# Kernel optimization log

Hardware: AMD Instinct MI355X
Metric: run time of the kernel (lower is better)

The kernel has to match this reference:

```python
import jax, jax.numpy as jnp
import numpy as np

N = 8192  # batch size
D = 256   # embedding dim


def setup_inputs() -> dict:
    key = jax.random.key(0)
    k1, k2 = jax.random.split(key)
    return {
        "embeddings": jax.random.normal(k1, (N, D), dtype=jnp.float32),
        "query_embeddings": jax.random.normal(k2, (N, D), dtype=jnp.float32),
    }


def _l2_normalize(x, eps=1e-8):
    # matches torch F.cosine_similarity: x / max(||x||, eps)
    n = jnp.sqrt(jnp.sum(x * x, axis=-1, keepdims=True))
    return x / jnp.maximum(n, eps)


def _cross_entropy(logits, targets):
    # mean CE; out-of-range targets clamp to last class (jit gather semantics)
    lse = jax.nn.logsumexp(logits, axis=1)
    t = jnp.clip(targets, 0, logits.shape[1] - 1)
    picked = jnp.take_along_axis(logits, t[:, None], axis=1)[:, 0]
    return jnp.mean(lse - picked)


def reference(embeddings, query_embeddings):
    n = embeddings.shape[0]
    # normalize once, then single NxN matmul (instead of NxNxD broadcast)
    sim = _l2_normalize(embeddings) @ _l2_normalize(query_embeddings).T  # (N, N)
    rows = jnp.arange(n)
    positives = jnp.diagonal(sim)[:, None]  # (N, 1)
    # off-diagonal gather: per row, column indices skipping the diagonal
    idx = jnp.arange(n - 1)
    cols = idx[None, :] + (idx[None, :] >= rows[:, None]).astype(jnp.int32)
    negatives = jnp.take_along_axis(sim, cols, axis=1)  # (N, N-1)
    loss_pos = _cross_entropy(positives, rows)
    loss_neg = _cross_entropy(-negatives, rows)
    return loss_pos + loss_neg
```

## Files before the change

### kernel.cpp

```cpp
#include <hip/hip_runtime.h>
#include <hip/hip_bf16.h>

#define NROWS 8192
#define DIM 256
#define NSPLIT 16
#define JSPAN (NROWS / NSPLIT)
#define NGRP (JSPAN / 16)
#define RPW 64
#define RPB 256
#define GRP_BYTES 8192

typedef __bf16 bf16x8 __attribute__((ext_vector_type(8)));
typedef float f32x4 __attribute__((ext_vector_type(4)));

#define NEG_LOG2E -1.4426950408889634f
#define NEG_LN2   -0.6931471805599453f

__global__ __launch_bounds__(256) void k_normalize_all(const float* __restrict__ emb,
                                                       const float* __restrict__ qry,
                                                       __hip_bfloat16* __restrict__ En,
                                                       __hip_bfloat16* __restrict__ Qn,
                                                       float* __restrict__ rowsum,
                                                       float* __restrict__ out) {
    if (blockIdx.x < 8)
        reinterpret_cast<float4*>(rowsum)[blockIdx.x * 256 + threadIdx.x] =
            float4{0.f, 0.f, 0.f, 0.f};
    if (blockIdx.x == 8 && threadIdx.x == 0) out[0] = 0.f;

    const int gr   = blockIdx.x * 4 + (threadIdx.x >> 6);
    const int lane = threadIdx.x & 63;
    const bool isE = (gr < NROWS);
    const float* in = isE ? emb : qry;
    const int row   = isE ? gr : gr - NROWS;
    const float scale = isE ? NEG_LOG2E : 1.0f;

    const float4 v = reinterpret_cast<const float4*>(in + (size_t)row * DIM)[lane];
    float ss = v.x * v.x + v.y * v.y + v.z * v.z + v.w * v.w;
#pragma unroll
    for (int m = 32; m >= 1; m >>= 1) ss += __shfl_xor(ss, m, 64);
    const float inv = scale / fmaxf(sqrtf(ss), 1e-8f);
    __hip_bfloat16 o[4];
    o[0] = __float2bfloat16(v.x * inv);
    o[1] = __float2bfloat16(v.y * inv);
    o[2] = __float2bfloat16(v.z * inv);
    o[3] = __float2bfloat16(v.w * inv);
    const ushort4 o8 = *reinterpret_cast<const ushort4*>(o);

    if (isE) {
        reinterpret_cast<ushort4*>(En + (size_t)row * DIM)[lane] = o8;
    } else {
        const int g = row >> 4, c = row & 15;
        char* dst = (char*)Qn + (size_t)g * GRP_BYTES
                    + (size_t)(lane >> 3) * 1024 + c * 64 + (lane & 7) * 8;
        *reinterpret_cast<ushort4*>(dst) = o8;
    }
}

__device__ __forceinline__ void stage_group(const char* qlane, char* wdst) {
#pragma unroll
    for (int kk = 0; kk < 8; ++kk)
        __builtin_amdgcn_global_load_lds(
            (const __attribute__((address_space(1))) void*)(qlane + kk * 1024),
            (__attribute__((address_space(3))) void*)(wdst + kk * 1024), 16, 0, 0);
}

__global__ __launch_bounds__(256, 2) void k_simlse(const __hip_bfloat16* __restrict__ En,
                                                   const __hip_bfloat16* __restrict__ Qn,
                                                   float* __restrict__ rowsum,
                                                   float* __restrict__ pickv) {
    __shared__ char lds[4][2][GRP_BYTES];
    const int bx   = blockIdx.x;
    const int ib   = bx >> 4;
    const int jq   = bx & 15;
    const int tid  = threadIdx.x;
    const int lane = tid & 63;
    const int w    = tid >> 6;
    const int l15  = lane & 15;
    const int lks  = lane >> 4;
    const int i0w  = ib * RPB + w * RPW;

    char* wbase = &lds[w][0][0];
    const char* rdbase = wbase + l15 * 64 + lks * 16;

    bf16x8 a[4][8];
    {
        const __hip_bfloat16* ab = En + (size_t)(i0w + l15) * DIM + lks * 8;
#pragma unroll
        for (int mi = 0; mi < 4; ++mi)
#pragma unroll
            for (int kk = 0; kk < 8; ++kk)
                a[mi][kk] = *reinterpret_cast<const bf16x8*>(ab + mi * 16 * DIM + kk * 32);
    }

    float racc[4][4];
#pragma unroll
    for (int mi = 0; mi < 4; ++mi)
#pragma unroll
        for (int r = 0; r < 4; ++r) racc[mi][r] = 0.0f;

    const int jq0 = jq * JSPAN;
    const char* qlane = (const char*)Qn + (size_t)jq0 * 512 + (size_t)lane * 16;
    const char* qnext = qlane + 2 * GRP_BYTES;

    auto step = [&](int p, int rdoff, const char* stsrc) {
        if (p == NGRP - 1) asm volatile("s_waitcnt vmcnt(0)" ::: "memory");
        else               asm volatile("s_waitcnt vmcnt(8)" ::: "memory");

        bf16x8 b[8];
#pragma unroll
        for (int kk = 0; kk < 8; ++kk)
            b[kk] = *reinterpret_cast<const bf16x8*>(rdbase + rdoff + kk * 1024);

        asm volatile("s_waitcnt lgkmcnt(0)" ::: "memory");

        if (p + 2 < NGRP) stage_group(stsrc, wbase + rdoff);

        f32x4 acc[4];
#pragma unroll
        for (int mi = 0; mi < 4; ++mi) acc[mi] = f32x4{0.f, 0.f, 0.f, 0.f};

        __builtin_amdgcn_s_setprio(1);
#pragma unroll
        for (int kk = 0; kk < 8; ++kk)
#pragma unroll
            for (int mi = 0; mi < 4; ++mi)
                acc[mi] = __builtin_amdgcn_mfma_f32_16x16x32_bf16(
                    a[mi][kk], b[kk], acc[mi], 0, 0, 0);
        __builtin_amdgcn_s_setprio(0);

        const int grpbase = jq0 + p * 16;
        const bool spec = (grpbase <= i0w + RPW) && (grpbase + 16 > i0w);
        if (!spec) {
#pragma unroll
            for (int mi = 0; mi < 4; ++mi)
#pragma unroll
                for (int r = 0; r < 4; ++r)
                    racc[mi][r] += __builtin_amdgcn_exp2f(acc[mi][r]);
        } else {
            const int jg = grpbase + l15;
#pragma unroll
            for (int mi = 0; mi < 4; ++mi) {
                const int ig0 = i0w + mi * 16 + lks * 4;
#pragma unroll
                for (int r = 0; r < 4; ++r) {
                    const float e  = __builtin_amdgcn_exp2f(acc[mi][r]);
                    const int   ig = ig0 + r;
                    racc[mi][r] += (jg == ig) ? 0.0f : e;
                    const int pc = (ig == NROWS - 1) ? (NROWS - 2) : (ig + 1);
                    if (jg == pc) pickv[ig] = acc[mi][r] * NEG_LN2;
                }
            }
        }
    };

    stage_group(qlane, wbase);
    stage_group(qlane + GRP_BYTES, wbase + GRP_BYTES);

    for (int pp = 0; pp < NGRP; pp += 2) {
        step(pp,     0,         qnext);
        step(pp + 1, GRP_BYTES, qnext + GRP_BYTES);
        qnext += 2 * GRP_BYTES;
    }

#pragma unroll
    for (int mi = 0; mi < 4; ++mi)
#pragma unroll
        for (int r = 0; r < 4; ++r) {
            float v = racc[mi][r];
            v += __shfl_xor(v, 1, 64);
            v += __shfl_xor(v, 2, 64);
            v += __shfl_xor(v, 4, 64);
            v += __shfl_xor(v, 8, 64);
            if (l15 == 0) atomicAdd(&rowsum[i0w + mi * 16 + lks * 4 + r], v);
        }
}

__global__ __launch_bounds__(256) void k_finalize(const float* __restrict__ rowsum,
                                                  const float* __restrict__ pickv,
                                                  float* __restrict__ out) {
    __shared__ float red[4];
    const int base = blockIdx.x * 512;
    float s = 0.0f;
#pragma unroll
    for (int it = 0; it < 2; ++it) {
        const int i = base + it * 256 + threadIdx.x;
        s += __logf(rowsum[i]) + pickv[i];
    }
#pragma unroll
    for (int m = 32; m >= 1; m >>= 1) s += __shfl_xor(s, m, 64);
    if ((threadIdx.x & 63) == 0) red[threadIdx.x >> 6] = s;
    __syncthreads();
    if (threadIdx.x == 0)
        atomicAdd(out, (red[0] + red[1] + red[2] + red[3]) * (1.0f / (float)NROWS));
}

extern "C" void kernel_launch(void* const* d_in, const int* in_sizes, int n_in,
                              void* d_out, int out_size, void* d_ws, size_t ws_size,
                              hipStream_t stream) {
    const float* emb = (const float*)d_in[0];
    const float* qry = (const float*)d_in[1];
    float* out = (float*)d_out;

    char* ws = (char*)d_ws;
    __hip_bfloat16* En = (__hip_bfloat16*)ws;
    __hip_bfloat16* Qn = (__hip_bfloat16*)(ws + (size_t)NROWS * DIM * 2);
    float* rowsum = (float*)(ws + (size_t)NROWS * DIM * 4);
    float* pickv  = rowsum + NROWS;

    k_normalize_all<<<2 * NROWS / 4, 256, 0, stream>>>(emb, qry, En, Qn, rowsum, out);
    k_simlse<<<32 * NSPLIT, 256, 0, stream>>>(En, Qn, rowsum, pickv);
    k_finalize<<<16, 256, 0, stream>>>(rowsum, pickv, out);
}
```

Measured before the change: 53.55 us.

## Switch similarity GEMM from bf16 to fp8 MFMA with repacked Q layout

Normalized embeddings and queries are now quantized to fp8 instead of bf16, and the similarity GEMM uses the fp8 16x16x32 MFMA. The Q staging layout, LDS group size, column split and occupancy hint are changed to match, and B fragments are now read from LDS inside the MFMA loop rather than preloaded. This halves operand bytes and uses the higher-throughput fp8 matrix path, but the exp of similarities computed from fp8 inputs loses precision, which may push the loss outside tolerance. The grid doubles to 1024 blocks, which adds more atomics on the row sums.

```diff
diff --git a/kernel.cpp b/kernel.cpp
--- a/kernel.cpp
+++ b/kernel.cpp
@@ -3,23 +3,23 @@
 
 #define NROWS 8192
 #define DIM 256
-#define NSPLIT 16
+#define NSPLIT 32
 #define JSPAN (NROWS / NSPLIT)
 #define NGRP (JSPAN / 16)
 #define RPW 64
 #define RPB 256
-#define GRP_BYTES 8192
-
-typedef __bf16 bf16x8 __attribute__((ext_vector_type(8)));
+#define GRP_BYTES 4096
+
 typedef float f32x4 __attribute__((ext_vector_type(4)));
+typedef long i64frag;
 
 #define NEG_LOG2E -1.4426950408889634f
 #define NEG_LN2   -0.6931471805599453f
 
 __global__ __launch_bounds__(256) void k_normalize_all(const float* __restrict__ emb,
                                                        const float* __restrict__ qry,
-                                                       __hip_bfloat16* __restrict__ En,
-                                                       __hip_bfloat16* __restrict__ Qn,
+                                                       unsigned char* __restrict__ En,
+                                                       unsigned char* __restrict__ Qn,
                                                        float* __restrict__ rowsum,
                                                        float* __restrict__ out) {
     if (blockIdx.x < 8)
@@ -39,39 +39,35 @@
 #pragma unroll
     for (int m = 32; m >= 1; m >>= 1) ss += __shfl_xor(ss, m, 64);
     const float inv = scale / fmaxf(sqrtf(ss), 1e-8f);
-    __hip_bfloat16 o[4];
-    o[0] = __float2bfloat16(v.x * inv);
-    o[1] = __float2bfloat16(v.y * inv);
-    o[2] = __float2bfloat16(v.z * inv);
-    o[3] = __float2bfloat16(v.w * inv);
-    const ushort4 o8 = *reinterpret_cast<const ushort4*>(o);
+
+    int pk = __builtin_amdgcn_cvt_pk_fp8_f32(v.x * inv, v.y * inv, 0, false);
+    pk     = __builtin_amdgcn_cvt_pk_fp8_f32(v.z * inv, v.w * inv, pk, true);
 
     if (isE) {
-        reinterpret_cast<ushort4*>(En + (size_t)row * DIM)[lane] = o8;
+        *reinterpret_cast<int*>(En + (size_t)row * 256 + lane * 4) = pk;
     } else {
         const int g = row >> 4, c = row & 15;
-        char* dst = (char*)Qn + (size_t)g * GRP_BYTES
-                    + (size_t)(lane >> 3) * 1024 + c * 64 + (lane & 7) * 8;
-        *reinterpret_cast<ushort4*>(dst) = o8;
+        *reinterpret_cast<int*>(Qn + (size_t)g * GRP_BYTES + (lane >> 3) * 512
+                                + ((lane >> 1) & 3) * 128 + c * 8 + (lane & 1) * 4) = pk;
     }
 }
 
 __device__ __forceinline__ void stage_group(const char* qlane, char* wdst) {
 #pragma unroll
-    for (int kk = 0; kk < 8; ++kk)
+    for (int i = 0; i < 4; ++i)
         __builtin_amdgcn_global_load_lds(
-            (const __attribute__((address_space(1))) void*)(qlane + kk * 1024),
-            (__attribute__((address_space(3))) void*)(wdst + kk * 1024), 16, 0, 0);
-}
-
-__global__ __launch_bounds__(256, 2) void k_simlse(const __hip_bfloat16* __restrict__ En,
-                                                   const __hip_bfloat16* __restrict__ Qn,
+            (const __attribute__((address_space(1))) void*)(qlane + i * 1024),
+            (__attribute__((address_space(3))) void*)(wdst + i * 1024), 16, 0, 0);
+}
+
+__global__ __launch_bounds__(256, 4) void k_simlse(const unsigned char* __restrict__ En,
+                                                   const unsigned char* __restrict__ Qn,
                                                    float* __restrict__ rowsum,
                                                    float* __restrict__ pickv) {
     __shared__ char lds[4][2][GRP_BYTES];
     const int bx   = blockIdx.x;
-    const int ib   = bx >> 4;
-    const int jq   = bx & 15;
+    const int ib   = bx >> 5;
+    const int jq   = bx & 31;
     const int tid  = threadIdx.x;
     const int lane = tid & 63;
     const int w    = tid >> 6;
@@ -80,16 +76,16 @@
     const int i0w  = ib * RPB + w * RPW;
 
     char* wbase = &lds[w][0][0];
-    const char* rdbase = wbase + l15 * 64 + lks * 16;
-
-    bf16x8 a[4][8];
+    const char* rdbase = wbase + lane * 8;
+
+    i64frag a[4][8];
     {
-        const __hip_bfloat16* ab = En + (size_t)(i0w + l15) * DIM + lks * 8;
+        const unsigned char* ab = En + (size_t)(i0w + l15) * 256 + lks * 8;
 #pragma unroll
         for (int mi = 0; mi < 4; ++mi)
 #pragma unroll
             for (int kk = 0; kk < 8; ++kk)
-                a[mi][kk] = *reinterpret_cast<const bf16x8*>(ab + mi * 16 * DIM + kk * 32);
+                a[mi][kk] = *reinterpret_cast<const i64frag*>(ab + mi * 16 * 256 + kk * 32);
     }
 
     float racc[4][4];
@@ -99,34 +95,30 @@
         for (int r = 0; r < 4; ++r) racc[mi][r] = 0.0f;
 
     const int jq0 = jq * JSPAN;
-    const char* qlane = (const char*)Qn + (size_t)jq0 * 512 + (size_t)lane * 16;
+    const char* qlane = (const char*)Qn + (size_t)jq0 * 256 + (size_t)lane * 16;
     const char* qnext = qlane + 2 * GRP_BYTES;
 
     auto step = [&](int p, int rdoff, const char* stsrc) {
         if (p == NGRP - 1) asm volatile("s_waitcnt vmcnt(0)" ::: "memory");
-        else               asm volatile("s_waitcnt vmcnt(8)" ::: "memory");
-
-        bf16x8 b[8];
-#pragma unroll
-        for (int kk = 0; kk < 8; ++kk)
-            b[kk] = *reinterpret_cast<const bf16x8*>(rdbase + rdoff + kk * 1024);
+        else               asm volatile("s_waitcnt vmcnt(4)" ::: "memory");
+
+        f32x4 acc[4];
+#pragma unroll
+        for (int mi = 0; mi < 4; ++mi) acc[mi] = f32x4{0.f, 0.f, 0.f, 0.f};
+
+        __builtin_amdgcn_s_setprio(1);
+#pragma unroll
+        for (int kk = 0; kk < 8; ++kk) {
+            const i64frag b = *reinterpret_cast<const i64frag*>(rdbase + rdoff + kk * 512);
+#pragma unroll
+            for (int mi = 0; mi < 4; ++mi)
+                acc[mi] = __builtin_amdgcn_mfma_f32_16x16x32_fp8_fp8(
+                    a[mi][kk], b, acc[mi], 0, 0, 0);
+        }
+        __builtin_amdgcn_s_setprio(0);
 
         asm volatile("s_waitcnt lgkmcnt(0)" ::: "memory");
-
         if (p + 2 < NGRP) stage_group(stsrc, wbase + rdoff);
-
-        f32x4 acc[4];
-#pragma unroll
-        for (int mi = 0; mi < 4; ++mi) acc[mi] = f32x4{0.f, 0.f, 0.f, 0.f};
-
-        __builtin_amdgcn_s_setprio(1);
-#pragma unroll
-        for (int kk = 0; kk < 8; ++kk)
-#pragma unroll
-            for (int mi = 0; mi < 4; ++mi)
-                acc[mi] = __builtin_amdgcn_mfma_f32_16x16x32_bf16(
-                    a[mi][kk], b[kk], acc[mi], 0, 0, 0);
-        __builtin_amdgcn_s_setprio(0);
 
         const int grpbase = jq0 + p * 16;
         const bool spec = (grpbase <= i0w + RPW) && (grpbase + 16 > i0w);
@@ -202,9 +194,9 @@
     float* out = (float*)d_out;
 
     char* ws = (char*)d_ws;
-    __hip_bfloat16* En = (__hip_bfloat16*)ws;
-    __hip_bfloat16* Qn = (__hip_bfloat16*)(ws + (size_t)NROWS * DIM * 2);
-    float* rowsum = (float*)(ws + (size_t)NROWS * DIM * 4);
+    unsigned char* En = (unsigned char*)ws;
+    unsigned char* Qn = (unsigned char*)(ws + (size_t)NROWS * 256);
+    float* rowsum = (float*)(ws + (size_t)2 * NROWS * 256);
     float* pickv  = rowsum + NROWS;
 
     k_normalize_all<<<2 * NROWS / 4, 256, 0, stream>>>(emb, qry, En, Qn, rowsum, out);
```

Measured after the change: 62.15 us. 16.1% more time.

## Load Q tiles directly into registers instead of staging through LDS

Applied to the files above, without the earlier changes.

Drops the LDS staging buffer and global_load_lds path for the Q operand. Each lane now loads its B fragments straight from global memory into registers, double-buffered across two register sets with manual vmcnt waits. This removes LDS traffic and lgkm waits but raises register pressure (64 extra VGPRs for B) and relies on cache hits, since lanes in different waves reload the same Q data from global/L2.

```diff
diff --git a/kernel.cpp b/kernel.cpp
--- a/kernel.cpp
+++ b/kernel.cpp
@@ -56,19 +56,10 @@
     }
 }
 
-__device__ __forceinline__ void stage_group(const char* qlane, char* wdst) {
-#pragma unroll
-    for (int kk = 0; kk < 8; ++kk)
-        __builtin_amdgcn_global_load_lds(
-            (const __attribute__((address_space(1))) void*)(qlane + kk * 1024),
-            (__attribute__((address_space(3))) void*)(wdst + kk * 1024), 16, 0, 0);
-}
-
 __global__ __launch_bounds__(256, 2) void k_simlse(const __hip_bfloat16* __restrict__ En,
                                                    const __hip_bfloat16* __restrict__ Qn,
                                                    float* __restrict__ rowsum,
                                                    float* __restrict__ pickv) {
-    __shared__ char lds[4][2][GRP_BYTES];
     const int bx   = blockIdx.x;
     const int ib   = bx >> 4;
     const int jq   = bx & 15;
@@ -79,9 +70,6 @@
     const int lks  = lane >> 4;
     const int i0w  = ib * RPB + w * RPW;
 
-    char* wbase = &lds[w][0][0];
-    const char* rdbase = wbase + l15 * 64 + lks * 16;
-
     bf16x8 a[4][8];
     {
         const __hip_bfloat16* ab = En + (size_t)(i0w + l15) * DIM + lks * 8;
@@ -99,22 +87,16 @@
         for (int r = 0; r < 4; ++r) racc[mi][r] = 0.0f;
 
     const int jq0 = jq * JSPAN;
-    const char* qlane = (const char*)Qn + (size_t)jq0 * 512 + (size_t)lane * 16;
-    const char* qnext = qlane + 2 * GRP_BYTES;
-
-    auto step = [&](int p, int rdoff, const char* stsrc) {
-        if (p == NGRP - 1) asm volatile("s_waitcnt vmcnt(0)" ::: "memory");
-        else               asm volatile("s_waitcnt vmcnt(8)" ::: "memory");
-
-        bf16x8 b[8];
+    const char* qlane = (const char*)Qn + (size_t)jq0 * 512 + l15 * 64 + lks * 16;
+
+    auto loadB = [&](bf16x8 (&b)[8], int p) {
+        const char* gp = qlane + (size_t)p * GRP_BYTES;
 #pragma unroll
         for (int kk = 0; kk < 8; ++kk)
-            b[kk] = *reinterpret_cast<const bf16x8*>(rdbase + rdoff + kk * 1024);
-
-        asm volatile("s_waitcnt lgkmcnt(0)" ::: "memory");
-
-        if (p + 2 < NGRP) stage_group(stsrc, wbase + rdoff);
-
+            b[kk] = *reinterpret_cast<const bf16x8*>(gp + kk * 1024);
+    };
+
+    auto step = [&](const bf16x8 (&b)[8], int p) {
         f32x4 acc[4];
 #pragma unroll
         for (int mi = 0; mi < 4; ++mi) acc[mi] = f32x4{0.f, 0.f, 0.f, 0.f};
@@ -153,13 +135,20 @@
         }
     };
 
-    stage_group(qlane, wbase);
-    stage_group(qlane + GRP_BYTES, wbase + GRP_BYTES);
+    bf16x8 bA[8], bB[8];
+    loadB(bA, 0);
+    loadB(bB, 1);
 
     for (int pp = 0; pp < NGRP; pp += 2) {
-        step(pp,     0,         qnext);
-        step(pp + 1, GRP_BYTES, qnext + GRP_BYTES);
-        qnext += 2 * GRP_BYTES;
+        if (pp == NGRP - 2) asm volatile("s_waitcnt vmcnt(8)" ::: "memory");
+        else                asm volatile("s_waitcnt vmcnt(8)" ::: "memory");
+        step(bA, pp);
+        if (pp + 2 < NGRP) loadB(bA, pp + 2);
+
+        if (pp + 2 < NGRP) asm volatile("s_waitcnt vmcnt(8)" ::: "memory");
+        else               asm volatile("s_waitcnt vmcnt(0)" ::: "memory");
+        step(bB, pp + 1);
+        if (pp + 3 < NGRP) loadB(bB, pp + 3);
     }
 
 #pragma unroll
```

Result: slower. 70.62 us (+31.9%).

## Share Q tiles across eight waves via block-wide double-buffered LDS staging

Applied to the files above, without the earlier changes.

Blocks grow from 4 to 8 waves (512 rows each). Instead of every wave staging its own private copy of the Q column groups, all waves now cooperatively load a shared 64-column tile into a double-buffered LDS area, with a block barrier between tiles. This cuts redundant global-to-LDS traffic by a factor of eight per block and halves the grid to 256 blocks. In exchange it adds block-wide barriers, lowers the number of blocks available to fill the GPU, and raises per-block LDS and register demand, which can limit how many blocks run per CU.

```diff
diff --git a/kernel.cpp b/kernel.cpp
--- a/kernel.cpp
+++ b/kernel.cpp
@@ -5,9 +5,11 @@
 #define DIM 256
 #define NSPLIT 16
 #define JSPAN (NROWS / NSPLIT)
-#define NGRP (JSPAN / 16)
+#define TILE_COLS 64
+#define TILE_BYTES (TILE_COLS * 512)
+#define NT (JSPAN / TILE_COLS)
 #define RPW 64
-#define RPB 256
+#define RPB 512
 #define GRP_BYTES 8192
 
 typedef __bf16 bf16x8 __attribute__((ext_vector_type(8)));
@@ -56,19 +58,11 @@
     }
 }
 
-__device__ __forceinline__ void stage_group(const char* qlane, char* wdst) {
-#pragma unroll
-    for (int kk = 0; kk < 8; ++kk)
-        __builtin_amdgcn_global_load_lds(
-            (const __attribute__((address_space(1))) void*)(qlane + kk * 1024),
-            (__attribute__((address_space(3))) void*)(wdst + kk * 1024), 16, 0, 0);
-}
-
-__global__ __launch_bounds__(256, 2) void k_simlse(const __hip_bfloat16* __restrict__ En,
+__global__ __launch_bounds__(512, 2) void k_simlse(const __hip_bfloat16* __restrict__ En,
                                                    const __hip_bfloat16* __restrict__ Qn,
                                                    float* __restrict__ rowsum,
                                                    float* __restrict__ pickv) {
-    __shared__ char lds[4][2][GRP_BYTES];
+    __shared__ char lds[2][TILE_BYTES];
     const int bx   = blockIdx.x;
     const int ib   = bx >> 4;
     const int jq   = bx & 15;
@@ -79,9 +73,6 @@
     const int lks  = lane >> 4;
     const int i0w  = ib * RPB + w * RPW;
 
-    char* wbase = &lds[w][0][0];
-    const char* rdbase = wbase + l15 * 64 + lks * 16;
-
     bf16x8 a[4][8];
     {
         const __hip_bfloat16* ab = En + (size_t)(i0w + l15) * DIM + lks * 8;
@@ -99,67 +90,80 @@
         for (int r = 0; r < 4; ++r) racc[mi][r] = 0.0f;
 
     const int jq0 = jq * JSPAN;
-    const char* qlane = (const char*)Qn + (size_t)jq0 * 512 + (size_t)lane * 16;
-    const char* qnext = qlane + 2 * GRP_BYTES;
-
-    auto step = [&](int p, int rdoff, const char* stsrc) {
-        if (p == NGRP - 1) asm volatile("s_waitcnt vmcnt(0)" ::: "memory");
-        else               asm volatile("s_waitcnt vmcnt(8)" ::: "memory");
-
-        bf16x8 b[8];
-#pragma unroll
-        for (int kk = 0; kk < 8; ++kk)
-            b[kk] = *reinterpret_cast<const bf16x8*>(rdbase + rdoff + kk * 1024);
-
-        asm volatile("s_waitcnt lgkmcnt(0)" ::: "memory");
-
-        if (p + 2 < NGRP) stage_group(stsrc, wbase + rdoff);
-
-        f32x4 acc[4];
-#pragma unroll
-        for (int mi = 0; mi < 4; ++mi) acc[mi] = f32x4{0.f, 0.f, 0.f, 0.f};
-
-        __builtin_amdgcn_s_setprio(1);
-#pragma unroll
-        for (int kk = 0; kk < 8; ++kk)
-#pragma unroll
-            for (int mi = 0; mi < 4; ++mi)
-                acc[mi] = __builtin_amdgcn_mfma_f32_16x16x32_bf16(
-                    a[mi][kk], b[kk], acc[mi], 0, 0, 0);
-        __builtin_amdgcn_s_setprio(0);
-
-        const int grpbase = jq0 + p * 16;
-        const bool spec = (grpbase <= i0w + RPW) && (grpbase + 16 > i0w);
-        if (!spec) {
-#pragma unroll
-            for (int mi = 0; mi < 4; ++mi)
-#pragma unroll
-                for (int r = 0; r < 4; ++r)
-                    racc[mi][r] += __builtin_amdgcn_exp2f(acc[mi][r]);
-        } else {
-            const int jg = grpbase + l15;
-#pragma unroll
-            for (int mi = 0; mi < 4; ++mi) {
-                const int ig0 = i0w + mi * 16 + lks * 4;
-#pragma unroll
-                for (int r = 0; r < 4; ++r) {
-                    const float e  = __builtin_amdgcn_exp2f(acc[mi][r]);
-                    const int   ig = ig0 + r;
-                    racc[mi][r] += (jg == ig) ? 0.0f : e;
-                    const int pc = (ig == NROWS - 1) ? (NROWS - 2) : (ig + 1);
-                    if (jg == pc) pickv[ig] = acc[mi][r] * NEG_LN2;
+    const char* qtile = (const char*)Qn + (size_t)jq0 * 512 + (size_t)lane * 16
+                        + (size_t)w * 4096;
+
+    auto stage_tile = [&](const char* src, char* buf) {
+#pragma unroll
+        for (int i = 0; i < 4; ++i)
+            __builtin_amdgcn_global_load_lds(
+                (const __attribute__((address_space(1))) void*)(src + i * 1024),
+                (__attribute__((address_space(3))) void*)(buf + w * 4096 + i * 1024),
+                16, 0, 0);
+    };
+
+    stage_tile(qtile, lds[0]);
+    asm volatile("s_waitcnt vmcnt(0)" ::: "memory");
+    __builtin_amdgcn_s_barrier();
+
+    for (int t = 0; t < NT; ++t) {
+        const char* cur = lds[t & 1];
+        char* nxt       = lds[(t + 1) & 1];
+        if (t + 1 < NT) stage_tile(qtile + TILE_BYTES, nxt);
+        qtile += TILE_BYTES;
+
+        const char* rd = cur + l15 * 64 + lks * 16;
+        const int tbase = jq0 + t * TILE_COLS;
+
+#pragma unroll
+        for (int g = 0; g < 4; ++g) {
+            bf16x8 b[8];
+#pragma unroll
+            for (int kk = 0; kk < 8; ++kk)
+                b[kk] = *reinterpret_cast<const bf16x8*>(rd + (g * 8 + kk) * 1024);
+
+            f32x4 acc[4];
+#pragma unroll
+            for (int mi = 0; mi < 4; ++mi) acc[mi] = f32x4{0.f, 0.f, 0.f, 0.f};
+
+            __builtin_amdgcn_s_setprio(1);
+#pragma unroll
+            for (int kk = 0; kk < 8; ++kk)
+#pragma unroll
+                for (int mi = 0; mi < 4; ++mi)
+                    acc[mi] = __builtin_amdgcn_mfma_f32_16x16x32_bf16(
+                        a[mi][kk], b[kk], acc[mi], 0, 0, 0);
+            __builtin_amdgcn_s_setprio(0);
+
+            const int grpbase = tbase + g * 16;
+            const bool spec = (grpbase <= i0w + RPW) && (grpbase + 16 > i0w);
+            if (!spec) {
+#pragma unroll
+                for (int mi = 0; mi < 4; ++mi)
+#pragma unroll
+                    for (int r = 0; r < 4; ++r)
+                        racc[mi][r] += __builtin_amdgcn_exp2f(acc[mi][r]);
+            } else {
+                const int jg = grpbase + l15;
+#pragma unroll
+                for (int mi = 0; mi < 4; ++mi) {
+                    const int ig0 = i0w + mi * 16 + lks * 4;
+#pragma unroll
+                    for (int r = 0; r < 4; ++r) {
+                        const float e  = __builtin_amdgcn_exp2f(acc[mi][r]);
+                        const int   ig = ig0 + r;
+                        racc[mi][r] += (jg == ig) ? 0.0f : e;
+                        const int pc = (ig == NROWS - 1) ? (NROWS - 2) : (ig + 1);
+                        if (jg == pc) pickv[ig] = acc[mi][r] * NEG_LN2;
+                    }
                 }
             }
         }
-    };
-
-    stage_group(qlane, wbase);
-    stage_group(qlane + GRP_BYTES, wbase + GRP_BYTES);
-
-    for (int pp = 0; pp < NGRP; pp += 2) {
-        step(pp,     0,         qnext);
-        step(pp + 1, GRP_BYTES, qnext + GRP_BYTES);
-        qnext += 2 * GRP_BYTES;
+
+        if (t + 1 < NT) {
+            asm volatile("s_waitcnt vmcnt(0)" ::: "memory");
+            __builtin_amdgcn_s_barrier();
+        }
     }
 
 #pragma unroll
@@ -208,6 +212,6 @@
     float* pickv  = rowsum + NROWS;
 
     k_normalize_all<<<2 * NROWS / 4, 256, 0, stream>>>(emb, qry, En, Qn, rowsum, out);
-    k_simlse<<<32 * NSPLIT, 256, 0, stream>>>(En, Qn, rowsum, pickv);
+    k_simlse<<<16 * NSPLIT, 512, 0, stream>>>(En, Qn, rowsum, pickv);
     k_finalize<<<16, 256, 0, stream>>>(rowsum, pickv, out);
 }
```

Result: faster. 50.97 us (-4.8%).
